# Optimization experiments

Hardware: AMD Instinct MI355X
Metric: run time of the kernel (lower is better)

The kernel has to match this reference:

```python
import jax, jax.numpy as jnp
import numpy as np

B, S, D, H = 2, 2048, 1024, 16
HD = D // H  # head_dim = 64


def setup_inputs() -> dict:
    key = jax.random.key(0)
    ks = jax.random.split(key, 12)
    scale = 1.0 / np.sqrt(D)
    inp = {
        "query": jax.random.normal(ks[0], (B, S, D), dtype=jnp.float32),
        "key_in": jax.random.normal(ks[1], (B, S, D), dtype=jnp.float32),
        "value": jax.random.normal(ks[2], (B, S, D), dtype=jnp.float32),
        "mask": jnp.zeros((B, S), dtype=bool),
        # nn.Linear weights stored as [out, in] like torch; y = x @ W.T + b
        "Wq": jax.random.normal(ks[3], (D, D), dtype=jnp.float32) * scale,
        "bq": jnp.zeros((D,), dtype=jnp.float32),
        "Wk": jax.random.normal(ks[4], (D, D), dtype=jnp.float32) * scale,
        "bk": jnp.zeros((D,), dtype=jnp.float32),
        "Wv": jax.random.normal(ks[5], (D, D), dtype=jnp.float32) * scale,
        "bv": jnp.zeros((D,), dtype=jnp.float32),
        "Wo": jax.random.normal(ks[6], (D, D), dtype=jnp.float32) * scale,
        "bo": jnp.zeros((D,), dtype=jnp.float32),
    }
    return inp


def reference(query, key_in, value, mask, Wq, bq, Wk, bk, Wv, bv, Wo, bo):
    def split_heads(x):  # [B,S,D] -> [B,H,S,HD]
        return x.reshape(B, -1, H, HD).transpose(0, 2, 1, 3)

    Q = split_heads(query @ Wq.T + bq)
    K = split_heads(key_in @ Wk.T + bk)
    V = split_heads(value @ Wv.T + bv)

    scores = jnp.einsum("bhqd,bhkd->bhqk", Q, K) / np.sqrt(HD)
    # key-padding mask: True -> -inf, broadcast over heads and query positions
    scores = jnp.where(mask[:, None, None, :], -jnp.inf, scores)
    attn = jax.nn.softmax(scores, axis=-1)
    out = jnp.einsum("bhqk,bhkd->bhqd", attn, V)  # [B,H,S,HD]
    out = out.transpose(0, 2, 1, 3).reshape(B, -1, D)
    return out @ Wo.T + bo
```

## Files before the change

kernel.cpp:

```cpp
#include <hip/hip_runtime.h>

typedef __attribute__((ext_vector_type(8))) __bf16 bf16x8;
typedef __attribute__((ext_vector_type(4))) float f32x4;
typedef __attribute__((ext_vector_type(16))) float f32x16;
typedef __attribute__((ext_vector_type(4))) unsigned int u32x4;
typedef __attribute__((ext_vector_type(8))) _Float16 f16x8;
typedef __attribute__((ext_vector_type(4))) _Float16 f16x4;
typedef unsigned short us;

#define SEQ 2048
#define DIM 1024
#define NH 16
#define HDIM 64

#define QSCALE 0.1803368801111204f

__device__ inline us f2bf(float f) {
    unsigned u = __builtin_bit_cast(unsigned, f);
    u += 0x7FFFu + ((u >> 16) & 1u);
    return (us)(u >> 16);
}

__device__ inline unsigned sx32(unsigned v) {
    return (unsigned)__shfl_xor((int)v, 32);
}

__device__ __forceinline__ size_t qk_idx(int bh, int s, int d) {
    return (((size_t)bh * 64 + (s >> 5)) << 11) + ((d >> 4) << 9)
         + (((s & 31) + (((d >> 3) & 1) << 5)) << 3) + (d & 7);
}
__device__ __forceinline__ size_t v_idx(int bh, int d, int s) {
    return (((size_t)bh * 64 + (s >> 5)) << 11) + ((((d >> 5) << 1) + ((s >> 4) & 1)) << 9)
         + (((d & 31) + (((s >> 3) & 1) << 5)) << 3) + (s & 7);
}

__device__ __forceinline__ void gload16(const us* g, us* l) {
    __builtin_amdgcn_global_load_lds(
        (const __attribute__((address_space(1))) unsigned int*)(const void*)g,
        (__attribute__((address_space(3))) unsigned int*)(void*)l, 16, 0, 0);
}

__global__ __launch_bounds__(256) void cast_many(
    const float* __restrict__ s0, const float* __restrict__ s1,
    const float* __restrict__ s2, const float* __restrict__ s3,
    us* __restrict__ dst, int n_each)
{
    const float* src = (blockIdx.y == 0) ? s0 : (blockIdx.y == 1) ? s1
                     : (blockIdx.y == 2) ? s2 : s3;
    size_t base = (size_t)blockIdx.y * (size_t)n_each;
    int i = (blockIdx.x * 256 + threadIdx.x) * 4;
    if (i < n_each) {
        float4 v = *(const float4*)(src + i);
        ushort4 o;
        o.x = f2bf(v.x); o.y = f2bf(v.y); o.z = f2bf(v.z); o.w = f2bf(v.w);
        *(ushort4*)(dst + base + i) = o;
    }
}

__global__ __launch_bounds__(64) void maskpack(
    const unsigned char* __restrict__ mask, unsigned* __restrict__ mw)
{
    int t = blockIdx.x * 64 + threadIdx.x;
    unsigned wv = 0;
#pragma unroll
    for (int j = 0; j < 32; j++) wv |= (mask[t * 32 + j] ? 1u : 0u) << j;
    mw[t] = wv;
}

#define BM 128
#define BN 128
#define BK 64

__device__ __forceinline__ void gemm_core(
    const us* __restrict__ A, const us* __restrict__ W,
    const float* __restrict__ bias, void* __restrict__ out,
    int M, int N, int K, int mode, float oscale)
{
    __shared__ us lA[BM * BK];
    __shared__ us lB[BN * BK];

    const int tid  = threadIdx.x;
    const int lane = tid & 63;
    const int w    = tid >> 6;
    const int wm   = w >> 1, wn = w & 1;
    const int m0   = blockIdx.y * BM, n0 = blockIdx.x * BN;
    const int g    = lane >> 4, li = lane & 15;

    const f32x4 fz = {0.f, 0.f, 0.f, 0.f};
    f32x4 acc[4][4];
#pragma unroll
    for (int i = 0; i < 4; i++)
#pragma unroll
        for (int j = 0; j < 4; j++) acc[i][j] = fz;

    for (int k0 = 0; k0 < K; k0 += BK) {
#pragma unroll
        for (int i = 0; i < 4; i++) {
            int v = tid + i * 256;
            int row = v >> 3, c8 = (v & 7) * 8;
            gload16(&A[(size_t)(m0 + row) * K + k0 + c8], &lA[v * 8]);
            gload16(&W[(size_t)(n0 + row) * K + k0 + c8], &lB[v * 8]);
        }
        __syncthreads();
#pragma unroll
        for (int kk = 0; kk < 2; kk++) {
            bf16x8 af[4], bfr[4];
#pragma unroll
            for (int i = 0; i < 4; i++)
                af[i] = *(const bf16x8*)&lA[(wm * 64 + i * 16 + li) * BK + kk * 32 + g * 8];
#pragma unroll
            for (int j = 0; j < 4; j++)
                bfr[j] = *(const bf16x8*)&lB[(wn * 64 + j * 16 + li) * BK + kk * 32 + g * 8];
#pragma unroll
            for (int i = 0; i < 4; i++)
#pragma unroll
                for (int j = 0; j < 4; j++)
                    acc[i][j] = __builtin_amdgcn_mfma_f32_16x16x32_bf16(
                        af[i], bfr[j], acc[i][j], 0, 0, 0);
        }
        __syncthreads();
    }

    const int r0 = g * 4;
#pragma unroll
    for (int i = 0; i < 4; i++) {
#pragma unroll
        for (int j = 0; j < 4; j++) {
            int col = n0 + wn * 64 + j * 16 + li;
            float bs = bias[col];
#pragma unroll
            for (int r = 0; r < 4; r++) {
                int row = m0 + wm * 64 + i * 16 + r0 + r;
                float val = (acc[i][j][r] + bs) * oscale;
                if (mode == 2) {
                    ((float*)out)[(size_t)row * N + col] = val;
                } else {
                    int s = row & (SEQ - 1);
                    int bh = ((row >> 11) << 4) + (col >> 6);
                    int d  = col & (HDIM - 1);
                    size_t idx = (mode == 0) ? qk_idx(bh, s, d) : v_idx(bh, d, s);
                    ((us*)out)[idx] = f2bf(val);
                }
            }
        }
    }
}

__global__ __launch_bounds__(256) void gemm_qkv(
    const us* __restrict__ xq, const us* __restrict__ xk, const us* __restrict__ xv,
    const us* __restrict__ wq, const us* __restrict__ wk, const us* __restrict__ wv,
    const float* __restrict__ bq, const float* __restrict__ bk, const float* __restrict__ bv,
    us* __restrict__ Qb, us* __restrict__ Kb, us* __restrict__ VTb)
{
    int z = blockIdx.z;
    if (z == 0)      gemm_core(xq, wq, bq, Qb,  2 * SEQ, DIM, DIM, 0, QSCALE);
    else if (z == 1) gemm_core(xk, wk, bk, Kb,  2 * SEQ, DIM, DIM, 0, 1.0f);
    else             gemm_core(xv, wv, bv, VTb, 2 * SEQ, DIM, DIM, 1, 1.0f);
}

__global__ __launch_bounds__(256) void gemm_one(
    const us* __restrict__ A, const us* __restrict__ W,
    const float* __restrict__ bias, float* __restrict__ out)
{
    gemm_core(A, W, bias, out, 2 * SEQ, DIM, DIM, 2, 1.0f);
}

__global__ __launch_bounds__(256, 4) void attn_split(
    const us* __restrict__ Qb, const us* __restrict__ Kb,
    const us* __restrict__ VT, const unsigned* __restrict__ mw,
    _Float16* __restrict__ opart, float* __restrict__ mlpart)
{
    const int tid  = threadIdx.x;
    const int w    = tid >> 6, lane = tid & 63;
    const int unit = blockIdx.x * 4 + w;
    const int tile = unit >> 1, half = unit & 1;
    const int bh   = tile >> 6, qt = tile & 63;
    const int b    = bh >> 4;
    const int q0   = qt * 32;
    const int ql   = lane & 31, hi = lane >> 5;
    const int kv0  = half * 1024, kv1 = kv0 + 1024;

    const us* Qf = Qb + (((size_t)bh * 64 + qt) << 11) + lane * 8;
    const us* Kf = Kb + (((size_t)bh * 64) << 11) + lane * 8;
    const us* Vf = VT + (((size_t)bh * 64) << 11) + lane * 8;

    bf16x8 qf[4];
#pragma unroll
    for (int t = 0; t < 4; t++) qf[t] = *(const bf16x8*)(Qf + t * 512);

    const f32x16 z16 = {0,0,0,0,0,0,0,0,0,0,0,0,0,0,0,0};
    f32x16 o0 = z16, o1 = z16;
    float mrun = -1e30f, lrun = 0.f;

    bf16x8 kf[4];
#pragma unroll
    for (int t = 0; t < 4; t++)
        kf[t] = *(const bf16x8*)(Kf + ((size_t)(kv0 >> 5) << 11) + t * 512);

    for (int kv = kv0; kv < kv1; kv += 32) {
        const size_t koff = (size_t)(kv >> 5) << 11;

        f32x16 s = z16;
#pragma unroll
        for (int t = 0; t < 4; t++)
            s = __builtin_amdgcn_mfma_f32_32x32x16_bf16(kf[t], qf[t], s, 0, 0, 0);

        if (kv + 32 < kv1) {
            const us* Kn = Kf + koff + 2048;
#pragma unroll
            for (int t = 0; t < 4; t++) kf[t] = *(const bf16x8*)(Kn + t * 512);
        }
        bf16x8 vf0[2], vf1[2];
#pragma unroll
        for (int t = 0; t < 2; t++) {
            vf0[t] = *(const bf16x8*)(Vf + koff + t * 512);
            vf1[t] = *(const bf16x8*)(Vf + koff + 1024 + t * 512);
        }

        unsigned m32 = (unsigned)__builtin_amdgcn_readfirstlane(
            (int)mw[b * 64 + (kv >> 5)]);

        float t8[8];
#pragma unroll
        for (int j = 0; j < 8; j++) t8[j] = fmaxf(s[j], s[j + 8]);
#pragma unroll
        for (int j = 0; j < 4; j++) t8[j] = fmaxf(t8[j], t8[j + 4]);
        float pmax = fmaxf(fmaxf(t8[0], t8[1]), fmaxf(t8[2], t8[3]));

        if (!__all(pmax <= mrun + 8.f)) {
            float pm = fmaxf(pmax, __shfl_xor(pmax, 32));
            float nm = fmaxf(mrun, pm);
            float corr = __builtin_amdgcn_exp2f(mrun - nm);
            lrun *= corr;
#pragma unroll
            for (int j = 0; j < 16; j++) { o0[j] *= corr; o1[j] *= corr; }
            mrun = nm;
        }

        float p[16];
#pragma unroll
        for (int r = 0; r < 16; r++) p[r] = __builtin_amdgcn_exp2f(s[r] - mrun);
        if (m32) {
            unsigned ms = hi ? (m32 >> 4) : m32;
#pragma unroll
            for (int r = 0; r < 16; r++)
                if ((ms >> ((r & 3) + 8 * (r >> 2))) & 1) p[r] = 0.f;
        }
        float a8[8];
#pragma unroll
        for (int j = 0; j < 8; j++) a8[j] = p[j] + p[j + 8];
#pragma unroll
        for (int j = 0; j < 4; j++) a8[j] += a8[j + 4];
        lrun += (a8[0] + a8[1]) + (a8[2] + a8[3]);

        unsigned pw[8];
#pragma unroll
        for (int j = 0; j < 8; j++)
            asm("v_cvt_pk_bf16_f32 %0, %1, %2"
                : "=v"(pw[j]) : "v"(p[2 * j]), "v"(p[2 * j + 1]));

        unsigned y0 = sx32(hi ? pw[0] : pw[2]);
        unsigned y1 = sx32(hi ? pw[1] : pw[3]);
        unsigned y2 = sx32(hi ? pw[4] : pw[6]);
        unsigned y3 = sx32(hi ? pw[5] : pw[7]);

        u32x4 t0, t1;
        t0.x = hi ? y0    : pw[0];
        t0.y = hi ? y1    : pw[1];
        t0.z = hi ? pw[2] : y0;
        t0.w = hi ? pw[3] : y1;
        t1.x = hi ? y2    : pw[4];
        t1.y = hi ? y3    : pw[5];
        t1.z = hi ? pw[6] : y2;
        t1.w = hi ? pw[7] : y3;
        bf16x8 pa0 = __builtin_bit_cast(bf16x8, t0);
        bf16x8 pa1 = __builtin_bit_cast(bf16x8, t1);

        o0 = __builtin_amdgcn_mfma_f32_32x32x16_bf16(vf0[0], pa0, o0, 0, 0, 0);
        o0 = __builtin_amdgcn_mfma_f32_32x32x16_bf16(vf0[1], pa1, o0, 0, 0, 0);
        o1 = __builtin_amdgcn_mfma_f32_32x32x16_bf16(vf1[0], pa0, o1, 0, 0, 0);
        o1 = __builtin_amdgcn_mfma_f32_32x32x16_bf16(vf1[1], pa1, o1, 0, 0, 0);
    }

    float lh  = lrun + __shfl_xor(lrun, 32);
    float inv = __builtin_amdgcn_rcpf(lh);

    size_t orow = (size_t)half * 65536 + (size_t)bh * SEQ + q0 + ql;
    _Float16* od = opart + orow * 64;
#pragma unroll
    for (int g2 = 0; g2 < 4; g2++) {
        f16x4 v0, v1;
#pragma unroll
        for (int j = 0; j < 4; j++) {
            v0[j] = (_Float16)(o0[4 * g2 + j] * inv);
            v1[j] = (_Float16)(o1[4 * g2 + j] * inv);
        }
        *(f16x4*)(od + 8 * g2 + 4 * hi)      = v0;
        *(f16x4*)(od + 32 + 8 * g2 + 4 * hi) = v1;
    }
    if (hi == 0) {
        float2 mlv; mlv.x = mrun; mlv.y = lh;
        *(float2*)&mlpart[orow * 2] = mlv;
    }
}

__global__ __launch_bounds__(256) void attn_combine(
    const _Float16* __restrict__ op, const float* __restrict__ ml,
    us* __restrict__ AO)
{
    int t   = blockIdx.x * 256 + threadIdx.x;
    int row = t >> 3, dc = (t & 7) * 8;
    int bh  = row >> 11, q = row & (SEQ - 1);
    int b   = bh >> 4, h = bh & 15;

    float2 ml0 = *(const float2*)&ml[(size_t)row * 2];
    float2 ml1 = *(const float2*)&ml[(size_t)(65536 + row) * 2];
    float M  = fmaxf(ml0.x, ml1.x);
    float w0 = ml0.y * __builtin_amdgcn_exp2f(ml0.x - M);
    float w1 = ml1.y * __builtin_amdgcn_exp2f(ml1.x - M);
    float wi = __builtin_amdgcn_rcpf(w0 + w1);
    float a0 = w0 * wi, a1 = w1 * wi;

    f16x8 v0 = *(const f16x8*)(op + (size_t)row * 64 + dc);
    f16x8 v1 = *(const f16x8*)(op + 4194304 + (size_t)row * 64 + dc);

    ushort4 r0, r1;
    r0.x = f2bf(a0 * (float)v0[0] + a1 * (float)v1[0]);
    r0.y = f2bf(a0 * (float)v0[1] + a1 * (float)v1[1]);
    r0.z = f2bf(a0 * (float)v0[2] + a1 * (float)v1[2]);
    r0.w = f2bf(a0 * (float)v0[3] + a1 * (float)v1[3]);
    r1.x = f2bf(a0 * (float)v0[4] + a1 * (float)v1[4]);
    r1.y = f2bf(a0 * (float)v0[5] + a1 * (float)v1[5]);
    r1.z = f2bf(a0 * (float)v0[6] + a1 * (float)v1[6]);
    r1.w = f2bf(a0 * (float)v0[7] + a1 * (float)v1[7]);

    us* dst = AO + ((size_t)b * SEQ + q) * DIM + h * HDIM + dc;
    *(ushort4*)dst       = r0;
    *(ushort4*)(dst + 4) = r1;
}

extern "C" void kernel_launch(void* const* d_in, const int* in_sizes, int n_in,
                              void* d_out, int out_size, void* d_ws, size_t ws_size,
                              hipStream_t stream)
{
    const float* q  = (const float*)d_in[0];
    const float* k  = (const float*)d_in[1];
    const float* v  = (const float*)d_in[2];
    const unsigned char* mask = (const unsigned char*)d_in[3];
    const float* Wq = (const float*)d_in[4];
    const float* bq = (const float*)d_in[5];
    const float* Wk = (const float*)d_in[6];
    const float* bk = (const float*)d_in[7];
    const float* Wv = (const float*)d_in[8];
    const float* bv = (const float*)d_in[9];
    const float* Wo = (const float*)d_in[10];
    const float* bo = (const float*)d_in[11];

    us* ws  = (us*)d_ws;
    us* xq  = ws;
    us* xk  = ws + 4194304;
    us* xv  = ws + 8388608;
    us* wqb = ws + 12582912;
    us* wkb = ws + 13631488;
    us* wvb = ws + 14680064;
    us* wob = ws + 15728640;
    us* Qb  = ws + 16777216;
    us* Kb  = ws + 20971520;
    us* VTb = ws + 25165824;
    us* AO  = ws + 29360128;
    unsigned* mwords = (unsigned*)(ws + 33554432);
    _Float16* opart  = (_Float16*)ws;
    float*    mlpart = (float*)(ws + 8388608 + 524288);

    cast_many<<<dim3(4096, 3), 256, 0, stream>>>(q, k, v, q, xq, 4194304);
    cast_many<<<dim3(1024, 4), 256, 0, stream>>>(Wq, Wk, Wv, Wo, wqb, 1048576);
    maskpack<<<dim3(2), 64, 0, stream>>>(mask, mwords);

    gemm_qkv<<<dim3(DIM / BN, (2 * SEQ) / BM, 3), 256, 0, stream>>>(
        xq, xk, xv, wqb, wkb, wvb, bq, bk, bv, Qb, Kb, VTb);

    attn_split<<<dim3(1024), 256, 0, stream>>>(Qb, Kb, VTb, mwords, opart, mlpart);
    attn_combine<<<dim3(2048), 256, 0, stream>>>(opart, mlpart, AO);

    gemm_one<<<dim3(DIM / BN, (2 * SEQ) / BM), 256, 0, stream>>>(AO, wob, bo, (float*)d_out);
}
```

Baseline: 263.7 us.

## Fuse cast and mask-pack launches and remap GEMM blocks across XCDs

Merges the two cast launches and the mask-pack launch into one prep kernel to remove two launch gaps. The QKV and output GEMMs switch to a flat 1D grid with a block remap, (L&7)*stride + (L>>3). This sends contiguous tiles to the same XCD on MI355X's round-robin dispatch, so neighbouring tiles can share L2 and reuse A/W rows. The risk is a small tail effect in the prep kernel, whose single mask block is mostly idle.

After: 263.9 us. No clear change (+0.1%).

```diff
diff --git a/kernel.cpp b/kernel.cpp
--- a/kernel.cpp
+++ b/kernel.cpp
@@ -40,31 +40,40 @@
         (__attribute__((address_space(3))) unsigned int*)(void*)l, 16, 0, 0);
 }
 
-__global__ __launch_bounds__(256) void cast_many(
-    const float* __restrict__ s0, const float* __restrict__ s1,
-    const float* __restrict__ s2, const float* __restrict__ s3,
-    us* __restrict__ dst, int n_each)
-{
-    const float* src = (blockIdx.y == 0) ? s0 : (blockIdx.y == 1) ? s1
-                     : (blockIdx.y == 2) ? s2 : s3;
-    size_t base = (size_t)blockIdx.y * (size_t)n_each;
-    int i = (blockIdx.x * 256 + threadIdx.x) * 4;
-    if (i < n_each) {
-        float4 v = *(const float4*)(src + i);
+__global__ __launch_bounds__(256) void prep(
+    const float* __restrict__ q, const float* __restrict__ k, const float* __restrict__ v,
+    const float* __restrict__ Wq, const float* __restrict__ Wk,
+    const float* __restrict__ Wv, const float* __restrict__ Wo,
+    const unsigned char* __restrict__ mask,
+    us* __restrict__ acts, us* __restrict__ wts, unsigned* __restrict__ mw)
+{
+    int bid = blockIdx.x, tid = threadIdx.x;
+    if (bid < 12288) {
+        int which = bid >> 12;
+        const float* src = (which == 0) ? q : (which == 1) ? k : v;
+        int i = ((bid & 4095) * 256 + tid) * 4;
+        float4 vv = *(const float4*)(src + i);
         ushort4 o;
-        o.x = f2bf(v.x); o.y = f2bf(v.y); o.z = f2bf(v.z); o.w = f2bf(v.w);
-        *(ushort4*)(dst + base + i) = o;
-    }
-}
-
-__global__ __launch_bounds__(64) void maskpack(
-    const unsigned char* __restrict__ mask, unsigned* __restrict__ mw)
-{
-    int t = blockIdx.x * 64 + threadIdx.x;
-    unsigned wv = 0;
-#pragma unroll
-    for (int j = 0; j < 32; j++) wv |= (mask[t * 32 + j] ? 1u : 0u) << j;
-    mw[t] = wv;
+        o.x = f2bf(vv.x); o.y = f2bf(vv.y); o.z = f2bf(vv.z); o.w = f2bf(vv.w);
+        *(ushort4*)(acts + (size_t)which * 4194304 + i) = o;
+    } else if (bid < 16384) {
+        int wb = bid - 12288;
+        int which = wb >> 10;
+        const float* src = (which == 0) ? Wq : (which == 1) ? Wk
+                         : (which == 2) ? Wv : Wo;
+        int i = ((wb & 1023) * 256 + tid) * 4;
+        float4 vv = *(const float4*)(src + i);
+        ushort4 o;
+        o.x = f2bf(vv.x); o.y = f2bf(vv.y); o.z = f2bf(vv.z); o.w = f2bf(vv.w);
+        *(ushort4*)(wts + (size_t)which * 1048576 + i) = o;
+    } else {
+        if (tid < 128) {
+            unsigned wv = 0;
+#pragma unroll
+            for (int j = 0; j < 32; j++) wv |= (mask[tid * 32 + j] ? 1u : 0u) << j;
+            mw[tid] = wv;
+        }
+    }
 }
 
 #define BM 128
@@ -74,7 +83,7 @@
 __device__ __forceinline__ void gemm_core(
     const us* __restrict__ A, const us* __restrict__ W,
     const float* __restrict__ bias, void* __restrict__ out,
-    int M, int N, int K, int mode, float oscale)
+    int m0, int n0, int mode, float oscale)
 {
     __shared__ us lA[BM * BK];
     __shared__ us lB[BN * BK];
@@ -83,8 +92,8 @@
     const int lane = tid & 63;
     const int w    = tid >> 6;
     const int wm   = w >> 1, wn = w & 1;
-    const int m0   = blockIdx.y * BM, n0 = blockIdx.x * BN;
     const int g    = lane >> 4, li = lane & 15;
+    const int K    = DIM, N = DIM;
 
     const f32x4 fz = {0.f, 0.f, 0.f, 0.f};
     f32x4 acc[4][4];
@@ -152,17 +161,24 @@
     const float* __restrict__ bq, const float* __restrict__ bk, const float* __restrict__ bv,
     us* __restrict__ Qb, us* __restrict__ Kb, us* __restrict__ VTb)
 {
-    int z = blockIdx.z;
-    if (z == 0)      gemm_core(xq, wq, bq, Qb,  2 * SEQ, DIM, DIM, 0, QSCALE);
-    else if (z == 1) gemm_core(xk, wk, bk, Kb,  2 * SEQ, DIM, DIM, 0, 1.0f);
-    else             gemm_core(xv, wv, bv, VTb, 2 * SEQ, DIM, DIM, 1, 1.0f);
+    int L    = blockIdx.x;
+    int orig = (L & 7) * 96 + (L >> 3);
+    int z    = orig >> 8;
+    int rem  = orig & 255;
+    int m0   = (rem >> 3) * BM, n0 = (rem & 7) * BN;
+    if (z == 0)      gemm_core(xq, wq, bq, Qb,  m0, n0, 0, QSCALE);
+    else if (z == 1) gemm_core(xk, wk, bk, Kb,  m0, n0, 0, 1.0f);
+    else             gemm_core(xv, wv, bv, VTb, m0, n0, 1, 1.0f);
 }
 
 __global__ __launch_bounds__(256) void gemm_one(
     const us* __restrict__ A, const us* __restrict__ W,
     const float* __restrict__ bias, float* __restrict__ out)
 {
-    gemm_core(A, W, bias, out, 2 * SEQ, DIM, DIM, 2, 1.0f);
+    int L    = blockIdx.x;
+    int orig = (L & 7) * 32 + (L >> 3);
+    int m0   = (orig >> 3) * BM, n0 = (orig & 7) * BN;
+    gemm_core(A, W, bias, out, m0, n0, 2, 1.0f);
 }
 
 __global__ __launch_bounds__(256, 4) void attn_split(
@@ -372,15 +388,14 @@
     _Float16* opart  = (_Float16*)ws;
     float*    mlpart = (float*)(ws + 8388608 + 524288);
 
-    cast_many<<<dim3(4096, 3), 256, 0, stream>>>(q, k, v, q, xq, 4194304);
-    cast_many<<<dim3(1024, 4), 256, 0, stream>>>(Wq, Wk, Wv, Wo, wqb, 1048576);
-    maskpack<<<dim3(2), 64, 0, stream>>>(mask, mwords);
-
-    gemm_qkv<<<dim3(DIM / BN, (2 * SEQ) / BM, 3), 256, 0, stream>>>(
+    prep<<<dim3(16385), 256, 0, stream>>>(q, k, v, Wq, Wk, Wv, Wo, mask,
+                                          xq, wqb, mwords);
+
+    gemm_qkv<<<dim3(768), 256, 0, stream>>>(
         xq, xk, xv, wqb, wkb, wvb, bq, bk, bv, Qb, Kb, VTb);
 
     attn_split<<<dim3(1024), 256, 0, stream>>>(Qb, Kb, VTb, mwords, opart, mlpart);
     attn_combine<<<dim3(2048), 256, 0, stream>>>(opart, mlpart, AO);
 
-    gemm_one<<<dim3(DIM / BN, (2 * SEQ) / BM), 256, 0, stream>>>(AO, wob, bo, (float*)d_out);
-}
+    gemm_one<<<dim3(256), 256, 0, stream>>>(AO, wob, bo, (float*)d_out);
+}
```
